# Kernel tuning notes

Measured on AMD Instinct MI355X. Metric: run time of the kernel, lower is better.

The kernel has to match this reference:

```python
import jax, jax.numpy as jnp
import numpy as np

TOP_K = 2  # module uses global top_k=2

def setup_inputs() -> dict:
    key = jax.random.key(0)
    k1, k2, k3 = jax.random.split(key, 3)
    B, S, D, E = 4, 4096, 2048, 64
    x = jax.random.normal(k1, (B, S, D), dtype=jnp.float32)
    W = jax.random.normal(k2, (E, D), dtype=jnp.float32) * 0.02  # gate_linear weight (no bias)
    noise_weight = jnp.zeros((E,), dtype=jnp.float32)  # nn.Parameter(torch.zeros(E))
    noise = jax.random.normal(k3, (B, S, E), dtype=jnp.float32)  # randn_like(logits) * noisy_std(=1.0)
    return {"x": x, "W": W, "noise_weight": noise_weight, "noise": noise}

def reference(x, W, noise_weight, noise):
    # logits = gate_linear(x)
    logits = jnp.einsum('bsd,ed->bse', x, W)
    # noisy logits: noise * noise_weight (per-expert scale), added to logits
    logits_noisy = logits + noise * noise_weight
    # top-k (largest, sorted descending, like torch.topk)
    top_vals, top_idx = jax.lax.top_k(logits_noisy, TOP_K)  # [B,S,k]
    B, S, E = logits_noisy.shape
    # scatter top-k values into -inf tensor along expert dim
    sparse = jnp.full_like(logits_noisy, -jnp.inf)
    b_ix = jnp.arange(B)[:, None, None]
    s_ix = jnp.arange(S)[None, :, None]
    sparse = sparse.at[b_ix, s_ix, top_idx].set(top_vals)
    # softmax over experts; exp(-inf)=0 zeros out non-selected experts
    gated_probs = jax.nn.softmax(sparse, axis=-1)
    return (gated_probs, top_idx, top_vals)
```

## Files before the change

### kernel.cpp

```cpp
#include <hip/hip_runtime.h>
#include <math.h>


typedef __attribute__((ext_vector_type(8))) __bf16 bf16x8;
typedef __attribute__((ext_vector_type(8))) unsigned short u16x8;
typedef __attribute__((ext_vector_type(4))) float f32x4;

constexpr int EXPN = 64;
constexpr int BM   = 32;
constexpr int BK   = 64;
constexpr int LDK  = BK + 8;

__device__ __forceinline__ void split2(float f, unsigned short& h, unsigned short& l) {
    const unsigned b = __float_as_uint(f);
    h = (unsigned short)(b >> 16);
    const float fh = __uint_as_float(b & 0xffff0000u);
    l = (unsigned short)(__float_as_uint(f - fh) >> 16);
}

__global__ __launch_bounds__(256)
void convert_w_kernel(const float* __restrict__ W,
                      unsigned short* __restrict__ whp,
                      unsigned short* __restrict__ wlp, int n4)
{
    const int i = blockIdx.x * 256 + threadIdx.x;
    if (i >= n4) return;
    const float4 v = *(const float4*)(W + (size_t)i * 4);
    const float f[4] = {v.x, v.y, v.z, v.w};
    unsigned short h[4], l[4];
#pragma unroll
    for (int j = 0; j < 4; ++j) split2(f[j], h[j], l[j]);
    *(ushort4*)(whp + (size_t)i * 4) = make_ushort4(h[0], h[1], h[2], h[3]);
    *(ushort4*)(wlp + (size_t)i * 4) = make_ushort4(l[0], l[1], l[2], l[3]);
}

__global__ __launch_bounds__(256)
void moe_gate_kernel(const float* __restrict__ x,
                     const float* __restrict__ W,
                     const unsigned short* __restrict__ whp,
                     const unsigned short* __restrict__ wlp,
                     const float* __restrict__ nw,
                     const float* __restrict__ noise,
                     float* __restrict__ probs,
                     float* __restrict__ idx_out,
                     float* __restrict__ val_out,
                     int D)
{
    __shared__ unsigned short xh[2][BM][LDK], xl[2][BM][LDK];
    __shared__ unsigned short wh[2][EXPN][LDK], wl[2][EXPN][LDK];
    __shared__ float ls[BM][EXPN + 1];

    const int tid  = threadIdx.x;
    const int lane = tid & 63;
    const int wv   = tid >> 6;
    const int hh   = wv & 1;
    const int qq   = wv >> 1;
    const int m0   = blockIdx.x * BM;

    const int xrow = tid >> 3;
    const int xcol = (tid & 7) * 8;
    const int wrow = tid >> 2;
    const int wcol = (tid & 3) * 16;

    const float*          xbase  = x   + (size_t)(m0 + xrow) * D + xcol;
    const unsigned short* whbase = whp + (size_t)wrow * D + wcol;
    const unsigned short* wlbase = wlp + (size_t)wrow * D + wcol;

    f32x4 acc0 = {0.f, 0.f, 0.f, 0.f};
    f32x4 acc1 = {0.f, 0.f, 0.f, 0.f};

    const int nchunk = D / BK;
    const int fr = lane & 15;
    const int kq = (lane >> 4) * 8;

    float4 ax0, ax1, bx0, bx1;
    u16x8  awh0, awh1, awl0, awl1, bwh0, bwh1, bwl0, bwl1;

#define LOAD_SET(X0, X1, WH0, WH1, WL0, WL1, ko)                        \
    X0  = *(const float4*)(xbase  + (ko));                              \
    X1  = *(const float4*)(xbase  + (ko) + 4);                          \
    WH0 = *(const u16x8*)(whbase + (ko));                               \
    WH1 = *(const u16x8*)(whbase + (ko) + 8);                           \
    WL0 = *(const u16x8*)(wlbase + (ko));                               \
    WL1 = *(const u16x8*)(wlbase + (ko) + 8);

#define STAGE_SET(X0, X1, WH0, WH1, WL0, WL1, b)                        \
    {                                                                   \
        const float xv_[8] = {X0.x, X0.y, X0.z, X0.w,                   \
                              X1.x, X1.y, X1.z, X1.w};                  \
        u16x8 hv_, lv_;                                                 \
        _Pragma("unroll")                                               \
        for (int i_ = 0; i_ < 8; ++i_) {                                \
            unsigned short a_, b_; split2(xv_[i_], a_, b_);             \
            hv_[i_] = a_; lv_[i_] = b_;                                 \
        }                                                               \
        *(u16x8*)&xh[b][xrow][xcol] = hv_;                              \
        *(u16x8*)&xl[b][xrow][xcol] = lv_;                              \
        *(u16x8*)&wh[b][wrow][wcol]     = WH0;                          \
        *(u16x8*)&wh[b][wrow][wcol + 8] = WH1;                          \
        *(u16x8*)&wl[b][wrow][wcol]     = WL0;                          \
        *(u16x8*)&wl[b][wrow][wcol + 8] = WL1;                          \
    }

#define MFMA_CHUNK(b)                                                   \
    _Pragma("unroll")                                                   \
    for (int ks = 0; ks < BK; ks += 32) {                               \
        const bf16x8 ah  = *(const bf16x8*)&xh[b][hh * 16 + fr][ks + kq]; \
        const bf16x8 al  = *(const bf16x8*)&xl[b][hh * 16 + fr][ks + kq]; \
        const bf16x8 b0h = *(const bf16x8*)&wh[b][qq * 32 + fr][ks + kq]; \
        const bf16x8 b0l = *(const bf16x8*)&wl[b][qq * 32 + fr][ks + kq]; \
        const bf16x8 b1h = *(const bf16x8*)&wh[b][qq * 32 + 16 + fr][ks + kq]; \
        const bf16x8 b1l = *(const bf16x8*)&wl[b][qq * 32 + 16 + fr][ks + kq]; \
        acc0 = __builtin_amdgcn_mfma_f32_16x16x32_bf16(ah, b0h, acc0, 0, 0, 0); \
        acc0 = __builtin_amdgcn_mfma_f32_16x16x32_bf16(ah, b0l, acc0, 0, 0, 0); \
        acc0 = __builtin_amdgcn_mfma_f32_16x16x32_bf16(al, b0h, acc0, 0, 0, 0); \
        acc1 = __builtin_amdgcn_mfma_f32_16x16x32_bf16(ah, b1h, acc1, 0, 0, 0); \
        acc1 = __builtin_amdgcn_mfma_f32_16x16x32_bf16(ah, b1l, acc1, 0, 0, 0); \
        acc1 = __builtin_amdgcn_mfma_f32_16x16x32_bf16(al, b1h, acc1, 0, 0, 0); \
    }

    LOAD_SET(ax0, ax1, awh0, awh1, awl0, awl1, 0)
    LOAD_SET(bx0, bx1, bwh0, bwh1, bwl0, bwl1, BK)

    for (int c = 0; c < nchunk; c += 2) {
        STAGE_SET(ax0, ax1, awh0, awh1, awl0, awl1, 0)
        __syncthreads();
        if (c + 2 < nchunk) {
            LOAD_SET(ax0, ax1, awh0, awh1, awl0, awl1, (c + 2) * BK)
        }
        MFMA_CHUNK(0)

        STAGE_SET(bx0, bx1, bwh0, bwh1, bwl0, bwl1, 1)
        __syncthreads();
        if (c + 3 < nchunk) {
            LOAD_SET(bx0, bx1, bwh0, bwh1, bwl0, bwl1, (c + 3) * BK)
        }
        MFMA_CHUNK(1)
    }

#undef LOAD_SET
#undef STAGE_SET
#undef MFMA_CHUNK

    const int trow = hh * 16 + (lane >> 4) * 4;
#pragma unroll
    for (int r = 0; r < 4; ++r) {
        ls[trow + r][qq * 32 + fr]      = acc0[r];
        ls[trow + r][qq * 32 + 16 + fr] = acc1[r];
    }
    __syncthreads();

    const float nwv = nw[lane];

#pragma unroll 1
    for (int t = 0; t < 8; ++t) {
        const int tl = wv * 8 + t;
        const int g  = m0 + tl;
        const float logit = fmaf(noise[(size_t)g * EXPN + lane], nwv, ls[tl][lane]);

        float v0; int i0;
        {
            float v = logit; int ix = lane;
#pragma unroll
            for (int off = 32; off; off >>= 1) {
                const float vo = __shfl_xor(v, off);
                const int   io = __shfl_xor(ix, off);
                if (vo > v || (vo == v && io < ix)) { v = vo; ix = io; }
            }
            v0 = v; i0 = ix;
        }
        float v1; int i1;
        {
            float v = (lane == i0) ? -INFINITY : logit; int ix = lane;
#pragma unroll
            for (int off = 32; off; off >>= 1) {
                const float vo = __shfl_xor(v, off);
                const int   io = __shfl_xor(ix, off);
                if (vo > v || (vo == v && io < ix)) { v = vo; ix = io; }
            }
            v1 = v; i1 = ix;
        }
        float v2; int i2;
        {
            float v = (lane == i0 || lane == i1) ? -INFINITY : logit; int ix = lane;
#pragma unroll
            for (int off = 32; off; off >>= 1) {
                const float vo = __shfl_xor(v, off);
                const int   io = __shfl_xor(ix, off);
                if (vo > v || (vo == v && io < ix)) { v = vo; ix = io; }
            }
            v2 = v; i2 = ix;
        }

        const float eps = 1e-3f;
        if ((v0 - v1) < eps || (v1 - v2) < eps) {
            const float* xr  = x + (size_t)g * D;
            const float* w0r = W + (size_t)i0 * D;
            const float* w1r = W + (size_t)i1 * D;
            const float* w2r = W + (size_t)i2 * D;
            double s0 = 0.0, s1 = 0.0, s2 = 0.0;
            for (int d = lane; d < D; d += 64) {
                const double xv = (double)xr[d];
                s0 += xv * (double)w0r[d];
                s1 += xv * (double)w1r[d];
                s2 += xv * (double)w2r[d];
            }
#pragma unroll
            for (int off = 32; off; off >>= 1) {
                s0 += __shfl_xor(s0, off);
                s1 += __shfl_xor(s1, off);
                s2 += __shfl_xor(s2, off);
            }
            double d0 = s0 + (double)noise[(size_t)g * EXPN + i0] * (double)nw[i0];
            double d1 = s1 + (double)noise[(size_t)g * EXPN + i1] * (double)nw[i1];
            double d2 = s2 + (double)noise[(size_t)g * EXPN + i2] * (double)nw[i2];
            #define CSWAP(va, ia, vb, ib)                                   \
                if ((vb > va) || (vb == va && ib < ia)) {                   \
                    double tv = va; va = vb; vb = tv;                       \
                    int ti = ia; ia = ib; ib = ti; }
            CSWAP(d0, i0, d1, i1)
            CSWAP(d1, i1, d2, i2)
            CSWAP(d0, i0, d1, i1)
            #undef CSWAP
            v0 = (float)d0; v1 = (float)d1;
        }

        const float e1  = expf(v1 - v0);
        const float inv = 1.0f / (1.0f + e1);

        float p = 0.f;
        if (lane == i0)      p = inv;
        else if (lane == i1) p = e1 * inv;
        probs[(size_t)g * EXPN + lane] = p;

        if (lane == 0) {
            idx_out[(size_t)g * 2 + 0] = (float)i0;
            idx_out[(size_t)g * 2 + 1] = (float)i1;
            val_out[(size_t)g * 2 + 0] = v0;
            val_out[(size_t)g * 2 + 1] = v1;
        }
    }
}

extern "C" void kernel_launch(void* const* d_in, const int* in_sizes, int n_in,
                              void* d_out, int out_size, void* d_ws, size_t ws_size,
                              hipStream_t stream) {
    const float* x     = (const float*)d_in[0];
    const float* W     = (const float*)d_in[1];
    const float* nw    = (const float*)d_in[2];
    const float* noise = (const float*)d_in[3];

    const int M = in_sizes[3] / EXPN;
    const int D = in_sizes[0] / M;
    const int wn = in_sizes[1];

    unsigned short* whp = (unsigned short*)d_ws;
    unsigned short* wlp = whp + (size_t)wn;

    float* probs   = (float*)d_out;
    float* idx_out = probs + (size_t)M * EXPN;
    float* val_out = idx_out + (size_t)M * 2;

    const int n4 = wn / 4;
    convert_w_kernel<<<(n4 + 255) / 256, 256, 0, stream>>>(W, whp, wlp, n4);

    const int grid = M / BM;
    moe_gate_kernel<<<grid, 256, 0, stream>>>(x, W, whp, wlp, nw, noise,
                                              probs, idx_out, val_out, D);
}
```

Measured before the change: 228.6 us.

## Drop LDS staging, load MFMA fragments directly from global with split-K across waves

Removes the shared-memory double-buffered staging of x and W. Each wave now loads its MFMA operands straight from global memory into registers, with a two-deep register prefetch. Tokens per block drop from 32 to 16, and the four waves split as two expert halves by two K halves, with the partial sums reduced through LDS at the end. This cuts LDS traffic and barriers and raises occupancy, at the cost of uncoalesced strided global loads and more global reads of the weight per token.

```diff
diff --git a/kernel.cpp b/kernel.cpp
--- a/kernel.cpp
+++ b/kernel.cpp
@@ -7,15 +7,17 @@
 typedef __attribute__((ext_vector_type(4))) float f32x4;
 
 constexpr int EXPN = 64;
-constexpr int BM   = 32;
-constexpr int BK   = 64;
-constexpr int LDK  = BK + 8;
+constexpr int TM   = 16;
 
 __device__ __forceinline__ void split2(float f, unsigned short& h, unsigned short& l) {
     const unsigned b = __float_as_uint(f);
     h = (unsigned short)(b >> 16);
     const float fh = __uint_as_float(b & 0xffff0000u);
     l = (unsigned short)(__float_as_uint(f - fh) >> 16);
+}
+
+__device__ __forceinline__ bf16x8 as_bf16(u16x8 v) {
+    union { u16x8 u; bf16x8 b; } c; c.u = v; return c.b;
 }
 
 __global__ __launch_bounds__(256)
@@ -34,7 +36,7 @@
     *(ushort4*)(wlp + (size_t)i * 4) = make_ushort4(l[0], l[1], l[2], l[3]);
 }
 
-__global__ __launch_bounds__(256)
+__global__ __launch_bounds__(256, 4)
 void moe_gate_kernel(const float* __restrict__ x,
                      const float* __restrict__ W,
                      const unsigned short* __restrict__ whp,
@@ -46,115 +48,100 @@
                      float* __restrict__ val_out,
                      int D)
 {
-    __shared__ unsigned short xh[2][BM][LDK], xl[2][BM][LDK];
-    __shared__ unsigned short wh[2][EXPN][LDK], wl[2][EXPN][LDK];
-    __shared__ float ls[BM][EXPN + 1];
+    __shared__ float ps[TM][EXPN + 1];
+    __shared__ float ls[TM][EXPN + 1];
 
     const int tid  = threadIdx.x;
     const int lane = tid & 63;
     const int wv   = tid >> 6;
-    const int hh   = wv & 1;
-    const int qq   = wv >> 1;
-    const int m0   = blockIdx.x * BM;
-
-    const int xrow = tid >> 3;
-    const int xcol = (tid & 7) * 8;
-    const int wrow = tid >> 2;
-    const int wcol = (tid & 3) * 16;
-
-    const float*          xbase  = x   + (size_t)(m0 + xrow) * D + xcol;
-    const unsigned short* whbase = whp + (size_t)wrow * D + wcol;
-    const unsigned short* wlbase = wlp + (size_t)wrow * D + wcol;
+    const int eh   = wv & 1;
+    const int kh   = wv >> 1;
+    const int m0   = blockIdx.x * TM;
+
+    const int fr = lane & 15;
+    const int kq = (lane >> 4) * 8;
+    const int khalf = D >> 1;
+    const int k0 = kh * khalf;
+
+    const float*          xb  = x   + (size_t)(m0 + fr) * D + k0 + kq;
+    const unsigned short* wh0 = whp + (size_t)(eh * 32 + fr)      * D + k0 + kq;
+    const unsigned short* wh1 = whp + (size_t)(eh * 32 + 16 + fr) * D + k0 + kq;
+    const unsigned short* wl0 = wlp + (size_t)(eh * 32 + fr)      * D + k0 + kq;
+    const unsigned short* wl1 = wlp + (size_t)(eh * 32 + 16 + fr) * D + k0 + kq;
 
     f32x4 acc0 = {0.f, 0.f, 0.f, 0.f};
     f32x4 acc1 = {0.f, 0.f, 0.f, 0.f};
 
-    const int nchunk = D / BK;
-    const int fr = lane & 15;
-    const int kq = (lane >> 4) * 8;
-
     float4 ax0, ax1, bx0, bx1;
-    u16x8  awh0, awh1, awl0, awl1, bwh0, bwh1, bwl0, bwl1;
-
-#define LOAD_SET(X0, X1, WH0, WH1, WL0, WL1, ko)                        \
-    X0  = *(const float4*)(xbase  + (ko));                              \
-    X1  = *(const float4*)(xbase  + (ko) + 4);                          \
-    WH0 = *(const u16x8*)(whbase + (ko));                               \
-    WH1 = *(const u16x8*)(whbase + (ko) + 8);                           \
-    WL0 = *(const u16x8*)(wlbase + (ko));                               \
-    WL1 = *(const u16x8*)(wlbase + (ko) + 8);
-
-#define STAGE_SET(X0, X1, WH0, WH1, WL0, WL1, b)                        \
+    u16x8  a0h, a0l, a1h, a1l, b0h, b0l, b1h, b1l;
+
+#define LOAD_SET(X0, X1, H0, L0, H1, L1, ko)                            \
+    X0 = *(const float4*)(xb  + (ko));                                  \
+    X1 = *(const float4*)(xb  + (ko) + 4);                              \
+    H0 = *(const u16x8*)(wh0 + (ko));                                   \
+    L0 = *(const u16x8*)(wl0 + (ko));                                   \
+    H1 = *(const u16x8*)(wh1 + (ko));                                   \
+    L1 = *(const u16x8*)(wl1 + (ko));
+
+#define COMPUTE(X0, X1, H0, L0, H1, L1)                                 \
     {                                                                   \
-        const float xv_[8] = {X0.x, X0.y, X0.z, X0.w,                   \
+        const float xf_[8] = {X0.x, X0.y, X0.z, X0.w,                   \
                               X1.x, X1.y, X1.z, X1.w};                  \
         u16x8 hv_, lv_;                                                 \
         _Pragma("unroll")                                               \
         for (int i_ = 0; i_ < 8; ++i_) {                                \
-            unsigned short a_, b_; split2(xv_[i_], a_, b_);             \
+            unsigned short a_, b_; split2(xf_[i_], a_, b_);             \
             hv_[i_] = a_; lv_[i_] = b_;                                 \
         }                                                               \
-        *(u16x8*)&xh[b][xrow][xcol] = hv_;                              \
-        *(u16x8*)&xl[b][xrow][xcol] = lv_;                              \
-        *(u16x8*)&wh[b][wrow][wcol]     = WH0;                          \
-        *(u16x8*)&wh[b][wrow][wcol + 8] = WH1;                          \
-        *(u16x8*)&wl[b][wrow][wcol]     = WL0;                          \
-        *(u16x8*)&wl[b][wrow][wcol + 8] = WL1;                          \
-    }
-
-#define MFMA_CHUNK(b)                                                   \
-    _Pragma("unroll")                                                   \
-    for (int ks = 0; ks < BK; ks += 32) {                               \
-        const bf16x8 ah  = *(const bf16x8*)&xh[b][hh * 16 + fr][ks + kq]; \
-        const bf16x8 al  = *(const bf16x8*)&xl[b][hh * 16 + fr][ks + kq]; \
-        const bf16x8 b0h = *(const bf16x8*)&wh[b][qq * 32 + fr][ks + kq]; \
-        const bf16x8 b0l = *(const bf16x8*)&wl[b][qq * 32 + fr][ks + kq]; \
-        const bf16x8 b1h = *(const bf16x8*)&wh[b][qq * 32 + 16 + fr][ks + kq]; \
-        const bf16x8 b1l = *(const bf16x8*)&wl[b][qq * 32 + 16 + fr][ks + kq]; \
-        acc0 = __builtin_amdgcn_mfma_f32_16x16x32_bf16(ah, b0h, acc0, 0, 0, 0); \
-        acc0 = __builtin_amdgcn_mfma_f32_16x16x32_bf16(ah, b0l, acc0, 0, 0, 0); \
-        acc0 = __builtin_amdgcn_mfma_f32_16x16x32_bf16(al, b0h, acc0, 0, 0, 0); \
-        acc1 = __builtin_amdgcn_mfma_f32_16x16x32_bf16(ah, b1h, acc1, 0, 0, 0); \
-        acc1 = __builtin_amdgcn_mfma_f32_16x16x32_bf16(ah, b1l, acc1, 0, 0, 0); \
-        acc1 = __builtin_amdgcn_mfma_f32_16x16x32_bf16(al, b1h, acc1, 0, 0, 0); \
-    }
-
-    LOAD_SET(ax0, ax1, awh0, awh1, awl0, awl1, 0)
-    LOAD_SET(bx0, bx1, bwh0, bwh1, bwl0, bwl1, BK)
-
-    for (int c = 0; c < nchunk; c += 2) {
-        STAGE_SET(ax0, ax1, awh0, awh1, awl0, awl1, 0)
-        __syncthreads();
-        if (c + 2 < nchunk) {
-            LOAD_SET(ax0, ax1, awh0, awh1, awl0, awl1, (c + 2) * BK)
-        }
-        MFMA_CHUNK(0)
-
-        STAGE_SET(bx0, bx1, bwh0, bwh1, bwl0, bwl1, 1)
-        __syncthreads();
-        if (c + 3 < nchunk) {
-            LOAD_SET(bx0, bx1, bwh0, bwh1, bwl0, bwl1, (c + 3) * BK)
-        }
-        MFMA_CHUNK(1)
+        const bf16x8 ah_ = as_bf16(hv_), al_ = as_bf16(lv_);            \
+        acc0 = __builtin_amdgcn_mfma_f32_16x16x32_bf16(ah_, as_bf16(H0), acc0, 0, 0, 0); \
+        acc0 = __builtin_amdgcn_mfma_f32_16x16x32_bf16(ah_, as_bf16(L0), acc0, 0, 0, 0); \
+        acc0 = __builtin_amdgcn_mfma_f32_16x16x32_bf16(al_, as_bf16(H0), acc0, 0, 0, 0); \
+        acc1 = __builtin_amdgcn_mfma_f32_16x16x32_bf16(ah_, as_bf16(H1), acc1, 0, 0, 0); \
+        acc1 = __builtin_amdgcn_mfma_f32_16x16x32_bf16(ah_, as_bf16(L1), acc1, 0, 0, 0); \
+        acc1 = __builtin_amdgcn_mfma_f32_16x16x32_bf16(al_, as_bf16(H1), acc1, 0, 0, 0); \
+    }
+
+    LOAD_SET(ax0, ax1, a0h, a0l, a1h, a1l, 0)
+    LOAD_SET(bx0, bx1, b0h, b0l, b1h, b1l, 32)
+
+    for (int ks = 0; ks < khalf; ks += 64) {
+        COMPUTE(ax0, ax1, a0h, a0l, a1h, a1l)
+        if (ks + 64 < khalf) {
+            LOAD_SET(ax0, ax1, a0h, a0l, a1h, a1l, ks + 64)
+        }
+        COMPUTE(bx0, bx1, b0h, b0l, b1h, b1l)
+        if (ks + 96 < khalf) {
+            LOAD_SET(bx0, bx1, b0h, b0l, b1h, b1l, ks + 96)
+        }
     }
 
 #undef LOAD_SET
-#undef STAGE_SET
-#undef MFMA_CHUNK
-
-    const int trow = hh * 16 + (lane >> 4) * 4;
-#pragma unroll
-    for (int r = 0; r < 4; ++r) {
-        ls[trow + r][qq * 32 + fr]      = acc0[r];
-        ls[trow + r][qq * 32 + 16 + fr] = acc1[r];
+#undef COMPUTE
+
+    const int trow = (lane >> 4) * 4;
+    if (kh == 1) {
+#pragma unroll
+        for (int r = 0; r < 4; ++r) {
+            ps[trow + r][eh * 32 + fr]      = acc0[r];
+            ps[trow + r][eh * 32 + 16 + fr] = acc1[r];
+        }
     }
     __syncthreads();
+    if (kh == 0) {
+#pragma unroll
+        for (int r = 0; r < 4; ++r) {
+            ls[trow + r][eh * 32 + fr]      = acc0[r] + ps[trow + r][eh * 32 + fr];
+            ls[trow + r][eh * 32 + 16 + fr] = acc1[r] + ps[trow + r][eh * 32 + 16 + fr];
+        }
+    }
+    __syncthreads();
 
     const float nwv = nw[lane];
 
 #pragma unroll 1
-    for (int t = 0; t < 8; ++t) {
-        const int tl = wv * 8 + t;
+    for (int t = 0; t < 4; ++t) {
+        const int tl = wv * 4 + t;
         const int g  = m0 + tl;
         const float logit = fmaf(noise[(size_t)g * EXPN + lane], nwv, ls[tl][lane]);
 
@@ -264,7 +251,7 @@
     const int n4 = wn / 4;
     convert_w_kernel<<<(n4 + 255) / 256, 256, 0, stream>>>(W, whp, wlp, n4);
 
-    const int grid = M / BM;
+    const int grid = M / TM;
     moe_gate_kernel<<<grid, 256, 0, stream>>>(x, W, whp, wlp, nw, noise,
                                               probs, idx_out, val_out, D);
 }
```

New measurement: 276.8 us. 1.21x slower.
